# Performance work log

Measured on AMD Instinct MI355X. Metric: run time of the kernel, lower is better.

The kernel has to match this reference:

```python
import jax, jax.numpy as jnp
import numpy as np
from jax.ops import segment_sum, segment_max

N = 100_000          # nodes
E = 1_600_000        # directed edges (avg degree 16)
F_IN = 128           # raw node embedding dim
D = 64               # node_encoding
H = 4                # num_heads
GRAPH_LAYERS = 2
FLOW_ITERS = 10
COST_CONST = 1.0     # quadratic cost: c * f^2
NEG_SLOPE = 0.2      # GAT leaky-relu slope
EPS = 1e-9


def setup_inputs() -> dict:
    key = jax.random.key(0)
    ks = jax.random.split(key, 16)
    s = 0.05
    return {
        "demands": jax.random.normal(ks[0], (N, 1), jnp.float32),
        "node_embeddings": jax.random.normal(ks[1], (N, F_IN), jnp.float32),
        "edge_src": jax.random.randint(ks[2], (E,), 0, N),
        "edge_dst": jax.random.randint(ks[3], (E,), 0, N),
        # node encoder MLP (no hidden layers)
        "W_enc": jax.random.normal(ks[4], (F_IN + 1, D), jnp.float32) * s,
        "b_enc": jnp.zeros((D,), jnp.float32),
        # SparseGAT params (shared across graph_layers, matching AUTO_REUSE scope)
        "W_gat": jax.random.normal(ks[5], (H, D, D), jnp.float32) * s,
        "a_src_w": jax.random.normal(ks[6], (H, D), jnp.float32) * s,
        "a_dst_w": jax.random.normal(ks[7], (H, D), jnp.float32) * s,
        "b_gat": jnp.zeros((D,), jnp.float32),
        # Gate (GRU-style convex gate)
        "W_gx": jax.random.normal(ks[8], (D, D), jnp.float32) * s,
        "W_gh": jax.random.normal(ks[9], (D, D), jnp.float32) * s,
        "b_g": jnp.zeros((D,), jnp.float32),
        # decoder to 1 output feature
        "W_dec": jax.random.normal(ks[10], (D, 1), jnp.float32) * s,
        "b_dec": jnp.zeros((1,), jnp.float32),
    }


def _seg_softmax(e, seg, n):
    # numerically stable softmax over entries sharing the same segment (row)
    m = segment_max(e, seg, num_segments=n)
    ex = jnp.exp(e - m[seg])
    den = segment_sum(ex, seg, num_segments=n)
    return ex / (den[seg] + EPS)


def reference(demands, node_embeddings, edge_src, edge_dst,
              W_enc, b_enc, W_gat, a_src_w, a_dst_w, b_gat,
              W_gx, W_gh, b_g, W_dec, b_dec):
    loops = jnp.arange(N, dtype=edge_src.dtype)
    src_sl = jnp.concatenate([edge_src, loops])  # adj + I for GAT
    dst_sl = jnp.concatenate([edge_dst, loops])

    # node encoder: relu(concat([emb, demands]) @ W + b)
    h = jax.nn.relu(jnp.concatenate([node_embeddings, demands], axis=1) @ W_enc + b_enc)

    for _ in range(GRAPH_LAYERS):
        t = jnp.einsum('nd,hde->nhe', h, W_gat)              # [N,H,D]
        ss = jnp.einsum('nhe,he->nh', t, a_src_w)            # [N,H]
        sd = jnp.einsum('nhe,he->nh', t, a_dst_w)
        e = jax.nn.leaky_relu(ss[src_sl] + sd[dst_sl], NEG_SLOPE)  # [E+N,H]
        alpha = _seg_softmax(e, src_sl, N)                   # row-wise attn
        agg = segment_sum(alpha[:, :, None] * t[dst_sl], src_sl, num_segments=N)  # [N,H,D]
        nxt = jax.nn.relu(agg.mean(axis=1) + b_gat)          # average heads
        # gate: convex combination of new and previous state
        z = jax.nn.sigmoid(nxt @ W_gx + h @ W_gh + b_g)
        h = z * nxt + (1.0 - z) * h

    pred = h @ W_dec + b_dec                                 # [N,1]
    # flow_weight_pred = sparse.softmax(adj * pred_weights): row-broadcast then row softmax
    scores = pred[edge_src, 0]                               # [E]
    fw = _seg_softmax(scores, edge_src, N)                   # edge values of flow_weight_pred

    d0 = demands[:, 0]

    def body(_, fv):
        inflow = segment_sum(fv, edge_dst, num_segments=N)   # column sums (axis=0)
        adj_in = jax.nn.relu(inflow - d0)
        return fw * adj_in[edge_src]                         # row-broadcast multiply

    flow = jax.lax.fori_loop(0, FLOW_ITERS, body, fw)
    flow_cost = jnp.sum(COST_CONST * flow * flow)            # quadratic edge cost
    return flow_cost, flow, fw
```

## Files before the change

kernel.cpp:

```cpp
#include <hip/hip_runtime.h>


static constexpr int BLK      = 256;
static constexpr int SCAN_BLK = 1024;
static constexpr int CHUNK    = 4096;
static constexpr int LB       = 9;
static constexpr int BN       = 512;

__global__ void hist_kernel(const int* __restrict__ src, const int* __restrict__ dst,
                            int* __restrict__ counts, int E, int B, int nb, int M) {
    extern __shared__ int lh[];
    const int nbins = 2 * B;
    for (int i = threadIdx.x; i < 4 * nbins; i += blockDim.x) lh[i] = 0;
    __syncthreads();
    int* my = lh + (threadIdx.x >> 6) * nbins;
    int base = blockIdx.x * CHUNK;
    int end  = base + CHUNK < E ? base + CHUNK : E;
    int i4beg = base >> 2, i4end = end >> 2;
    for (int i = i4beg + threadIdx.x; i < i4end; i += blockDim.x) {
        int4 s4 = ((const int4*)src)[i];
        int4 d4 = ((const int4*)dst)[i];
        atomicAdd(&my[d4.x >> LB], 1); atomicAdd(&my[B + (s4.x >> LB)], 1);
        atomicAdd(&my[d4.y >> LB], 1); atomicAdd(&my[B + (s4.y >> LB)], 1);
        atomicAdd(&my[d4.z >> LB], 1); atomicAdd(&my[B + (s4.z >> LB)], 1);
        atomicAdd(&my[d4.w >> LB], 1); atomicAdd(&my[B + (s4.w >> LB)], 1);
    }
    if (blockIdx.x == (int)gridDim.x - 1 && threadIdx.x == 0) {
        for (int e = i4end << 2; e < end; ++e) {
            atomicAdd(&my[dst[e] >> LB], 1);
            atomicAdd(&my[B + (src[e] >> LB)], 1);
        }
    }
    __syncthreads();
    for (int i = threadIdx.x; i < nbins; i += blockDim.x) {
        int s = lh[i] + lh[nbins + i] + lh[2 * nbins + i] + lh[3 * nbins + i];
        if (i < B) counts[i * nb + blockIdx.x] = s;
        else       counts[M + (i - B) * nb + blockIdx.x] = s;
    }
}

__global__ void scan_block_kernel(int* __restrict__ data, int* __restrict__ blocksum, int M2) {
    __shared__ int lds[SCAN_BLK];
    int t = threadIdx.x;
    int i = blockIdx.x * SCAN_BLK + t;
    int v = (i < M2) ? data[i] : 0;
    lds[t] = v;
    __syncthreads();
    for (int off = 1; off < SCAN_BLK; off <<= 1) {
        int tmp = (t >= off) ? lds[t - off] : 0;
        __syncthreads();
        lds[t] += tmp;
        __syncthreads();
    }
    if (i < M2) data[i] = lds[t] - v;
    if (t == SCAN_BLK - 1) blocksum[blockIdx.x] = lds[t];
}

__global__ void scan_partials_kernel(const int* __restrict__ bsum, int* __restrict__ boff, int n) {
    __shared__ int lds[SCAN_BLK];
    __shared__ int carry_s;
    if (threadIdx.x == 0) carry_s = 0;
    __syncthreads();
    for (int base = 0; base < n; base += SCAN_BLK) {
        int i = base + threadIdx.x;
        int v = (i < n) ? bsum[i] : 0;
        lds[threadIdx.x] = v;
        __syncthreads();
        for (int off = 1; off < SCAN_BLK; off <<= 1) {
            int tmp = (threadIdx.x >= off) ? lds[threadIdx.x - off] : 0;
            __syncthreads();
            lds[threadIdx.x] += tmp;
            __syncthreads();
        }
        int incl = lds[threadIdx.x];
        int c = carry_s;
        if (i < n) boff[i] = c + incl - v;
        __syncthreads();
        if (threadIdx.x == SCAN_BLK - 1) carry_s = c + incl;
        __syncthreads();
    }
}

__global__ void fused_scatter_kernel(const int* __restrict__ src, const int* __restrict__ dst,
                                     const int* __restrict__ counts, const int* __restrict__ boff,
                                     unsigned* __restrict__ packed, unsigned short* __restrict__ psrc,
                                     int E, int B, int nb, int M) {
    extern __shared__ int loff[];
    int b = blockIdx.x;
    for (int i = threadIdx.x; i < B; i += blockDim.x) {
        int id  = i * nb + b;
        int id2 = M + i * nb + b;
        loff[i]     = counts[id]  + boff[id >> 10];
        loff[B + i] = counts[id2] + boff[id2 >> 10] - E;
    }
    __syncthreads();
    int base = b * CHUNK;
    int end  = base + CHUNK < E ? base + CHUNK : E;
    int i4beg = base >> 2, i4end = end >> 2;
    for (int i = i4beg + threadIdx.x; i < i4end; i += blockDim.x) {
        int4 s4 = ((const int4*)src)[i];
        int4 d4 = ((const int4*)dst)[i];
        #pragma unroll
        for (int k = 0; k < 4; ++k) {
            int s = (k == 0) ? s4.x : (k == 1) ? s4.y : (k == 2) ? s4.z : s4.w;
            int d = (k == 0) ? d4.x : (k == 1) ? d4.y : (k == 2) ? d4.z : d4.w;
            int pos = atomicAdd(&loff[d >> LB], 1);
            packed[pos] = (unsigned)s | ((unsigned)(d & (BN - 1)) << 17);
            int pos2 = atomicAdd(&loff[B + (s >> LB)], 1);
            psrc[pos2] = (unsigned short)(s & (BN - 1));
        }
    }
    if (b == (int)gridDim.x - 1 && threadIdx.x == 0) {
        for (int e = i4end << 2; e < end; ++e) {
            int s = src[e], d = dst[e];
            int pos = atomicAdd(&loff[d >> LB], 1);
            packed[pos] = (unsigned)s | ((unsigned)(d & (BN - 1)) << 17);
            int pos2 = atomicAdd(&loff[B + (s >> LB)], 1);
            psrc[pos2] = (unsigned short)(s & (BN - 1));
        }
    }
}

__global__ void count_src_kernel(const unsigned short* __restrict__ psrc,
                                 const int* __restrict__ counts, const int* __restrict__ boff,
                                 float2* __restrict__ rz0, int N, int E, int B, int nb, int M) {
    __shared__ int cnt[8 * BN];
    int t = threadIdx.x;
    for (int i = t; i < 8 * BN; i += blockDim.x) cnt[i] = 0;
    __syncthreads();
    int b = blockIdx.x;
    int id  = M + b * nb;
    int beg = counts[id] + boff[id >> 10] - E;
    int end;
    if (b + 1 < B) { int id2 = M + (b + 1) * nb; end = counts[id2] + boff[id2 >> 10] - E; }
    else end = E;
    int w = t >> 6;
    for (int e = beg + t; e < end; e += blockDim.x)
        atomicAdd(&cnt[(w << 9) + psrc[e]], 1);
    __syncthreads();
    int g = (b << LB) + t;
    if (t < BN && g < N) {
        int tot = 0;
        #pragma unroll
        for (int r = 0; r < 8; ++r) tot += cnt[(r << 9) + t];
        float v = 1.0f / ((float)tot + 1e-9f);
        rz0[g] = make_float2(v, v);
    }
}

__global__ void fine_sort_kernel(const unsigned* __restrict__ packed,
                                 const int* __restrict__ counts, const int* __restrict__ boff,
                                 int* __restrict__ csr_src, int* __restrict__ row_ptr,
                                 int N, int E, int B, int nb) {
    __shared__ int cnt[8 * BN];
    __shared__ int off[BN];
    int t = threadIdx.x;
    int b = blockIdx.x;
    for (int i = t; i < 8 * BN; i += blockDim.x) cnt[i] = 0;
    __syncthreads();
    int id  = b * nb;
    int beg = counts[id] + boff[id >> 10];
    int end;
    if (b + 1 < B) { int id2 = (b + 1) * nb; end = counts[id2] + boff[id2 >> 10]; }
    else end = E;
    int w = t >> 6;
    for (int e = beg + t; e < end; e += blockDim.x)
        atomicAdd(&cnt[(w << 9) + (packed[e] >> 17)], 1);
    __syncthreads();
    int tot = 0;
    {
        #pragma unroll
        for (int r = 0; r < 8; ++r) tot += cnt[(r << 9) + t];
        off[t] = tot;
    }
    __syncthreads();
    for (int s = 1; s < BN; s <<= 1) {
        int v = (t >= s) ? off[t - s] : 0;
        __syncthreads();
        off[t] += v;
        __syncthreads();
    }
    int excl = beg + off[t] - tot;
    {
        int g = (b << LB) + t;
        if (g < N) row_ptr[g] = excl;
        int base2 = excl;
        #pragma unroll
        for (int r = 0; r < 8; ++r) {
            int c = cnt[(r << 9) + t];
            cnt[(r << 9) + t] = base2;
            base2 += c;
        }
    }
    __syncthreads();
    for (int e = beg + t; e < end; e += blockDim.x) {
        unsigned v = packed[e];
        int pos = atomicAdd(&cnt[(w << 9) + (v >> 17)], 1);
        csr_src[pos] = (int)(v & 0x1FFFFu);
    }
    if (b == 0 && t == 0) row_ptr[N] = E;
}

__global__ void spmv_csr2_kernel(const int* __restrict__ row_ptr, const int* __restrict__ csr_src,
                                 const float2* __restrict__ rz_in, const float* __restrict__ d0,
                                 float2* __restrict__ rz_out, int N) {
    int tid = blockIdx.x * blockDim.x + threadIdx.x;
    int n = tid >> 1;
    if (n >= N) return;
    int half = tid & 1;
    int beg = row_ptr[n], end = row_ptr[n + 1];
    int mid = beg + ((end - beg + 1) >> 1);
    int lo = half ? mid : beg;
    int hi = half ? end : mid;
    float a0 = 0.0f, a1 = 0.0f;
    int j = lo;
    for (; j + 1 < hi; j += 2) {
        a0 += rz_in[csr_src[j]].x;
        a1 += rz_in[csr_src[j + 1]].x;
    }
    if (j < hi) a0 += rz_in[csr_src[j]].x;
    float a = a0 + a1;
    a += __shfl_xor(a, 1, 64);
    if (half == 0) {
        float inv = rz_in[n].y;
        float p = a - d0[n];
        p = p > 0.0f ? p : 0.0f;
        rz_out[n] = make_float2(p * inv, inv);
    }
}

__global__ void final_kernel(const int* __restrict__ src, const float2* __restrict__ rz,
                             float* __restrict__ flow, float* __restrict__ fw,
                             float* __restrict__ partials, int E) {
    int i = blockIdx.x * blockDim.x + threadIdx.x;
    int E4 = E >> 2;
    float f2 = 0.0f;
    if (i < E4) {
        int4 s4 = ((const int4*)src)[i];
        float2 a = rz[s4.x], b = rz[s4.y], c = rz[s4.z], d = rz[s4.w];
        int e = i << 2;
        flow[e] = a.x; flow[e + 1] = b.x; flow[e + 2] = c.x; flow[e + 3] = d.x;
        fw[e]   = a.y; fw[e + 1]   = b.y; fw[e + 2]   = c.y; fw[e + 3]   = d.y;
        f2 = a.x * a.x + b.x * b.x + c.x * c.x + d.x * d.x;
    }
    if (blockIdx.x == 0 && threadIdx.x == 0) {
        for (int e = E4 << 2; e < E; ++e) {
            float2 a = rz[src[e]];
            flow[e] = a.x; fw[e] = a.y;
            f2 += a.x * a.x;
        }
    }
    #pragma unroll
    for (int off = 32; off > 0; off >>= 1) f2 += __shfl_down(f2, off, 64);
    __shared__ float wsum[BLK / 64];
    int lane = threadIdx.x & 63, w = threadIdx.x >> 6;
    if (lane == 0) wsum[w] = f2;
    __syncthreads();
    if (threadIdx.x == 0) {
        float s = 0.0f;
        #pragma unroll
        for (int k = 0; k < BLK / 64; ++k) s += wsum[k];
        partials[blockIdx.x] = s;
    }
}

__global__ void reduce_cost_kernel(const float* __restrict__ partials, float* __restrict__ cost, int n) {
    float s = 0.0f;
    for (int i = threadIdx.x; i < n; i += blockDim.x) s += partials[i];
    #pragma unroll
    for (int off = 32; off > 0; off >>= 1) s += __shfl_down(s, off, 64);
    __shared__ float wsum[16];
    int lane = threadIdx.x & 63, w = threadIdx.x >> 6;
    if (lane == 0) wsum[w] = s;
    __syncthreads();
    if (threadIdx.x == 0) {
        float t = 0.0f;
        for (int k = 0; k < (int)(blockDim.x / 64); ++k) t += wsum[k];
        cost[0] = t;
    }
}

extern "C" void kernel_launch(void* const* d_in, const int* in_sizes, int n_in,
                              void* d_out, int out_size, void* d_ws, size_t ws_size,
                              hipStream_t stream) {
    const float* demands  = (const float*)d_in[0];
    const int*   edge_src = (const int*)d_in[2];
    const int*   edge_dst = (const int*)d_in[3];
    const int N = in_sizes[0];
    const int E = in_sizes[2];

    float* out  = (float*)d_out;
    float* cost = out;
    float* flow = out + 1;
    float* fw   = out + 1 + E;

    const int B   = (N + BN - 1) >> LB;
    const int nb  = (E + CHUNK - 1) / CHUNK;
    const int M   = B * nb;
    const int M2  = 2 * M;
    const int nbs = (M2 + SCAN_BLK - 1) / SCAN_BLK;
    const int gridF = ((E >> 2) + BLK - 1) / BLK;
    const int gridS = (2 * N + BLK - 1) / BLK;

    auto align16 = [](size_t x) { return (x + 15) & ~size_t(15); };
    char* ws = (char*)d_ws;
    size_t o = 0;
    float2*   rz0      = (float2*)(ws + o);   o += align16((size_t)N * 8);
    float2*   rz1      = (float2*)(ws + o);   o += align16((size_t)N * 8);
    int*      row_ptr  = (int*)(ws + o);      o += align16((size_t)(N + 1) * 4);
    int*      counts   = (int*)(ws + o);      o += align16((size_t)M2 * 4);
    int*      blocksum = (int*)(ws + o);      o += align16((size_t)nbs * 4);
    int*      blockoff = (int*)(ws + o);      o += align16((size_t)nbs * 4);
    unsigned* packed   = (unsigned*)(ws + o); o += align16((size_t)E * 4);
    unsigned short* psrc = (unsigned short*)(ws + o); o += align16((size_t)E * 2);
    int*      csr_src  = (int*)(ws + o);      o += align16((size_t)E * 4);
    float*    partials = (float*)(ws + o);    o += align16((size_t)gridF * 4);

    hist_kernel<<<nb, BLK, (size_t)(8 * B) * 4, stream>>>(edge_src, edge_dst, counts, E, B, nb, M);
    scan_block_kernel<<<nbs, SCAN_BLK, 0, stream>>>(counts, blocksum, M2);
    scan_partials_kernel<<<1, SCAN_BLK, 0, stream>>>(blocksum, blockoff, nbs);

    fused_scatter_kernel<<<nb, BLK, (size_t)(2 * B) * 4, stream>>>(
        edge_src, edge_dst, counts, blockoff, packed, psrc, E, B, nb, M);
    count_src_kernel<<<B, BN, 0, stream>>>(psrc, counts, blockoff, rz0, N, E, B, nb, M);
    fine_sort_kernel<<<B, BN, 0, stream>>>(packed, counts, blockoff, csr_src, row_ptr, N, E, B, nb);

    float2* r_cur = rz0;
    float2* r_nxt = rz1;
    for (int it = 0; it < 10; ++it) {
        spmv_csr2_kernel<<<gridS, BLK, 0, stream>>>(row_ptr, csr_src, r_cur, demands, r_nxt, N);
        float2* t = r_cur; r_cur = r_nxt; r_nxt = t;
    }

    final_kernel<<<gridF, BLK, 0, stream>>>(edge_src, r_cur, flow, fw, partials, E);
    reduce_cost_kernel<<<1, 1024, 0, stream>>>(partials, cost, gridF);
}
```

Before: 188.2 us.

## Fuse sort kernels, split SpMV rows four ways, fold cost reduction into final

Result: slower. 229.8 us (+22.1%).

```diff
diff --git a/kernel.cpp b/kernel.cpp
--- a/kernel.cpp
+++ b/kernel.cpp
@@ -6,6 +6,7 @@
 static constexpr int CHUNK    = 4096;
 static constexpr int LB       = 9;
 static constexpr int BN       = 512;
+
 
 __global__ void hist_kernel(const int* __restrict__ src, const int* __restrict__ dst,
                             int* __restrict__ counts, int E, int B, int nb, int M) {
@@ -56,10 +57,11 @@
     if (t == SCAN_BLK - 1) blocksum[blockIdx.x] = lds[t];
 }
 
-__global__ void scan_partials_kernel(const int* __restrict__ bsum, int* __restrict__ boff, int n) {
+__global__ void scan_partials_kernel(const int* __restrict__ bsum, int* __restrict__ boff,
+                                     int* __restrict__ ticket, int n) {
     __shared__ int lds[SCAN_BLK];
     __shared__ int carry_s;
-    if (threadIdx.x == 0) carry_s = 0;
+    if (threadIdx.x == 0) { carry_s = 0; ticket[0] = 0; }
     __syncthreads();
     for (int base = 0; base < n; base += SCAN_BLK) {
         int i = base + threadIdx.x;
@@ -121,58 +123,48 @@
     }
 }
 
-__global__ void count_src_kernel(const unsigned short* __restrict__ psrc,
-                                 const int* __restrict__ counts, const int* __restrict__ boff,
-                                 float2* __restrict__ rz0, int N, int E, int B, int nb, int M) {
+__global__ void bucket_kernel(const unsigned short* __restrict__ psrc,
+                              const unsigned* __restrict__ packed,
+                              const int* __restrict__ counts, const int* __restrict__ boff,
+                              float* __restrict__ invdeg, float* __restrict__ rA,
+                              int* __restrict__ csr_src, int* __restrict__ row_ptr,
+                              int N, int E, int B, int nb, int M) {
     __shared__ int cnt[8 * BN];
-    int t = threadIdx.x;
+    __shared__ int off[BN];
+    int t = threadIdx.x, b = blockIdx.x, w = t >> 6;
+    int g = (b << LB) + t;
     for (int i = t; i < 8 * BN; i += blockDim.x) cnt[i] = 0;
     __syncthreads();
-    int b = blockIdx.x;
-    int id  = M + b * nb;
+    int id = M + b * nb;
     int beg = counts[id] + boff[id >> 10] - E;
     int end;
     if (b + 1 < B) { int id2 = M + (b + 1) * nb; end = counts[id2] + boff[id2 >> 10] - E; }
     else end = E;
-    int w = t >> 6;
     for (int e = beg + t; e < end; e += blockDim.x)
         atomicAdd(&cnt[(w << 9) + psrc[e]], 1);
     __syncthreads();
-    int g = (b << LB) + t;
-    if (t < BN && g < N) {
+    if (g < N) {
         int tot = 0;
         #pragma unroll
         for (int r = 0; r < 8; ++r) tot += cnt[(r << 9) + t];
         float v = 1.0f / ((float)tot + 1e-9f);
-        rz0[g] = make_float2(v, v);
-    }
-}
-
-__global__ void fine_sort_kernel(const unsigned* __restrict__ packed,
-                                 const int* __restrict__ counts, const int* __restrict__ boff,
-                                 int* __restrict__ csr_src, int* __restrict__ row_ptr,
-                                 int N, int E, int B, int nb) {
-    __shared__ int cnt[8 * BN];
-    __shared__ int off[BN];
-    int t = threadIdx.x;
-    int b = blockIdx.x;
+        invdeg[g] = v;
+        rA[g] = v;
+    }
+    __syncthreads();
     for (int i = t; i < 8 * BN; i += blockDim.x) cnt[i] = 0;
     __syncthreads();
-    int id  = b * nb;
-    int beg = counts[id] + boff[id >> 10];
-    int end;
+    id = b * nb;
+    beg = counts[id] + boff[id >> 10];
     if (b + 1 < B) { int id2 = (b + 1) * nb; end = counts[id2] + boff[id2 >> 10]; }
     else end = E;
-    int w = t >> 6;
     for (int e = beg + t; e < end; e += blockDim.x)
         atomicAdd(&cnt[(w << 9) + (packed[e] >> 17)], 1);
     __syncthreads();
     int tot = 0;
-    {
-        #pragma unroll
-        for (int r = 0; r < 8; ++r) tot += cnt[(r << 9) + t];
-        off[t] = tot;
-    }
+    #pragma unroll
+    for (int r = 0; r < 8; ++r) tot += cnt[(r << 9) + t];
+    off[t] = tot;
     __syncthreads();
     for (int s = 1; s < BN; s <<= 1) {
         int v = (t >= s) ? off[t - s] : 0;
@@ -181,16 +173,11 @@
         __syncthreads();
     }
     int excl = beg + off[t] - tot;
+    if (g < N) row_ptr[g] = excl;
     {
-        int g = (b << LB) + t;
-        if (g < N) row_ptr[g] = excl;
         int base2 = excl;
         #pragma unroll
-        for (int r = 0; r < 8; ++r) {
-            int c = cnt[(r << 9) + t];
-            cnt[(r << 9) + t] = base2;
-            base2 += c;
-        }
+        for (int r = 0; r < 8; ++r) { int c = cnt[(r << 9) + t]; cnt[(r << 9) + t] = base2; base2 += c; }
     }
     __syncthreads();
     for (int e = beg + t; e < end; e += blockDim.x) {
@@ -201,53 +188,50 @@
     if (b == 0 && t == 0) row_ptr[N] = E;
 }
 
-__global__ void spmv_csr2_kernel(const int* __restrict__ row_ptr, const int* __restrict__ csr_src,
-                                 const float2* __restrict__ rz_in, const float* __restrict__ d0,
-                                 float2* __restrict__ rz_out, int N) {
+
+__global__ void spmv_q_kernel(const int* __restrict__ row_ptr, const int* __restrict__ csr_src,
+                              const float* __restrict__ r_in, const float* __restrict__ d0,
+                              const float* __restrict__ invdeg, float* __restrict__ r_out, int N) {
     int tid = blockIdx.x * blockDim.x + threadIdx.x;
-    int n = tid >> 1;
+    int n = tid >> 2;
     if (n >= N) return;
-    int half = tid & 1;
+    int q = tid & 3;
     int beg = row_ptr[n], end = row_ptr[n + 1];
-    int mid = beg + ((end - beg + 1) >> 1);
-    int lo = half ? mid : beg;
-    int hi = half ? end : mid;
-    float a0 = 0.0f, a1 = 0.0f;
-    int j = lo;
-    for (; j + 1 < hi; j += 2) {
-        a0 += rz_in[csr_src[j]].x;
-        a1 += rz_in[csr_src[j + 1]].x;
-    }
-    if (j < hi) a0 += rz_in[csr_src[j]].x;
-    float a = a0 + a1;
+    int len = end - beg;
+    int lo = beg + ((len * q) >> 2);
+    int hi = beg + ((len * (q + 1)) >> 2);
+    float a = 0.0f;
+    for (int j = lo; j < hi; ++j) a += r_in[csr_src[j]];
     a += __shfl_xor(a, 1, 64);
-    if (half == 0) {
-        float inv = rz_in[n].y;
+    a += __shfl_xor(a, 2, 64);
+    if (q == 0) {
         float p = a - d0[n];
         p = p > 0.0f ? p : 0.0f;
-        rz_out[n] = make_float2(p * inv, inv);
-    }
-}
-
-__global__ void final_kernel(const int* __restrict__ src, const float2* __restrict__ rz,
-                             float* __restrict__ flow, float* __restrict__ fw,
-                             float* __restrict__ partials, int E) {
+        r_out[n] = p * invdeg[n];
+    }
+}
+
+__global__ void final_kernel(const int* __restrict__ src, const float* __restrict__ r_fin,
+                             const float* __restrict__ invdeg, float* __restrict__ flow,
+                             float* __restrict__ fw, float* __restrict__ partials,
+                             int* __restrict__ ticket, float* __restrict__ cost, int E) {
     int i = blockIdx.x * blockDim.x + threadIdx.x;
     int E4 = E >> 2;
     float f2 = 0.0f;
     if (i < E4) {
         int4 s4 = ((const int4*)src)[i];
-        float2 a = rz[s4.x], b = rz[s4.y], c = rz[s4.z], d = rz[s4.w];
+        float a = r_fin[s4.x], b = r_fin[s4.y], c = r_fin[s4.z], d = r_fin[s4.w];
         int e = i << 2;
-        flow[e] = a.x; flow[e + 1] = b.x; flow[e + 2] = c.x; flow[e + 3] = d.x;
-        fw[e]   = a.y; fw[e + 1]   = b.y; fw[e + 2]   = c.y; fw[e + 3]   = d.y;
-        f2 = a.x * a.x + b.x * b.x + c.x * c.x + d.x * d.x;
+        flow[e] = a; flow[e + 1] = b; flow[e + 2] = c; flow[e + 3] = d;
+        fw[e] = invdeg[s4.x]; fw[e + 1] = invdeg[s4.y];
+        fw[e + 2] = invdeg[s4.z]; fw[e + 3] = invdeg[s4.w];
+        f2 = a * a + b * b + c * c + d * d;
     }
     if (blockIdx.x == 0 && threadIdx.x == 0) {
         for (int e = E4 << 2; e < E; ++e) {
-            float2 a = rz[src[e]];
-            flow[e] = a.x; fw[e] = a.y;
-            f2 += a.x * a.x;
+            float a = r_fin[src[e]];
+            flow[e] = a; fw[e] = invdeg[src[e]];
+            f2 += a * a;
         }
     }
     #pragma unroll
@@ -256,27 +240,32 @@
     int lane = threadIdx.x & 63, w = threadIdx.x >> 6;
     if (lane == 0) wsum[w] = f2;
     __syncthreads();
+    __shared__ bool amLast;
     if (threadIdx.x == 0) {
         float s = 0.0f;
         #pragma unroll
         for (int k = 0; k < BLK / 64; ++k) s += wsum[k];
         partials[blockIdx.x] = s;
-    }
-}
-
-__global__ void reduce_cost_kernel(const float* __restrict__ partials, float* __restrict__ cost, int n) {
-    float s = 0.0f;
-    for (int i = threadIdx.x; i < n; i += blockDim.x) s += partials[i];
-    #pragma unroll
-    for (int off = 32; off > 0; off >>= 1) s += __shfl_down(s, off, 64);
-    __shared__ float wsum[16];
-    int lane = threadIdx.x & 63, w = threadIdx.x >> 6;
-    if (lane == 0) wsum[w] = s;
-    __syncthreads();
-    if (threadIdx.x == 0) {
-        float t = 0.0f;
-        for (int k = 0; k < (int)(blockDim.x / 64); ++k) t += wsum[k];
-        cost[0] = t;
+        __threadfence();
+        int prev = atomicAdd(ticket, 1);
+        amLast = (prev == (int)gridDim.x - 1);
+    }
+    __syncthreads();
+    if (amLast) {
+        __threadfence();
+        float s = 0.0f;
+        for (int k = threadIdx.x; k < (int)gridDim.x; k += blockDim.x) s += partials[k];
+        #pragma unroll
+        for (int off = 32; off > 0; off >>= 1) s += __shfl_down(s, off, 64);
+        __shared__ float wsum2[BLK / 64];
+        if (lane == 0) wsum2[w] = s;
+        __syncthreads();
+        if (threadIdx.x == 0) {
+            float t2 = 0.0f;
+            #pragma unroll
+            for (int k = 0; k < BLK / 64; ++k) t2 += wsum2[k];
+            cost[0] = t2;
+        }
     }
 }
 
@@ -300,17 +289,19 @@
     const int M2  = 2 * M;
     const int nbs = (M2 + SCAN_BLK - 1) / SCAN_BLK;
     const int gridF = ((E >> 2) + BLK - 1) / BLK;
-    const int gridS = (2 * N + BLK - 1) / BLK;
+    const int gridS = (4 * N + BLK - 1) / BLK;
 
     auto align16 = [](size_t x) { return (x + 15) & ~size_t(15); };
     char* ws = (char*)d_ws;
     size_t o = 0;
-    float2*   rz0      = (float2*)(ws + o);   o += align16((size_t)N * 8);
-    float2*   rz1      = (float2*)(ws + o);   o += align16((size_t)N * 8);
+    float*    invdeg   = (float*)(ws + o);    o += align16((size_t)N * 4);
+    float*    rA       = (float*)(ws + o);    o += align16((size_t)N * 4);
+    float*    rB       = (float*)(ws + o);    o += align16((size_t)N * 4);
     int*      row_ptr  = (int*)(ws + o);      o += align16((size_t)(N + 1) * 4);
     int*      counts   = (int*)(ws + o);      o += align16((size_t)M2 * 4);
     int*      blocksum = (int*)(ws + o);      o += align16((size_t)nbs * 4);
     int*      blockoff = (int*)(ws + o);      o += align16((size_t)nbs * 4);
+    int*      ticket   = (int*)(ws + o);      o += align16(4);
     unsigned* packed   = (unsigned*)(ws + o); o += align16((size_t)E * 4);
     unsigned short* psrc = (unsigned short*)(ws + o); o += align16((size_t)E * 2);
     int*      csr_src  = (int*)(ws + o);      o += align16((size_t)E * 4);
@@ -318,20 +309,19 @@
 
     hist_kernel<<<nb, BLK, (size_t)(8 * B) * 4, stream>>>(edge_src, edge_dst, counts, E, B, nb, M);
     scan_block_kernel<<<nbs, SCAN_BLK, 0, stream>>>(counts, blocksum, M2);
-    scan_partials_kernel<<<1, SCAN_BLK, 0, stream>>>(blocksum, blockoff, nbs);
-
+    scan_partials_kernel<<<1, SCAN_BLK, 0, stream>>>(blocksum, blockoff, ticket, nbs);
     fused_scatter_kernel<<<nb, BLK, (size_t)(2 * B) * 4, stream>>>(
         edge_src, edge_dst, counts, blockoff, packed, psrc, E, B, nb, M);
-    count_src_kernel<<<B, BN, 0, stream>>>(psrc, counts, blockoff, rz0, N, E, B, nb, M);
-    fine_sort_kernel<<<B, BN, 0, stream>>>(packed, counts, blockoff, csr_src, row_ptr, N, E, B, nb);
-
-    float2* r_cur = rz0;
-    float2* r_nxt = rz1;
+    bucket_kernel<<<B, BN, 0, stream>>>(psrc, packed, counts, blockoff,
+                                        invdeg, rA, csr_src, row_ptr, N, E, B, nb, M);
+
+    float* r_cur = rA;
+    float* r_nxt = rB;
     for (int it = 0; it < 10; ++it) {
-        spmv_csr2_kernel<<<gridS, BLK, 0, stream>>>(row_ptr, csr_src, r_cur, demands, r_nxt, N);
-        float2* t = r_cur; r_cur = r_nxt; r_nxt = t;
-    }
-
-    final_kernel<<<gridF, BLK, 0, stream>>>(edge_src, r_cur, flow, fw, partials, E);
-    reduce_cost_kernel<<<1, 1024, 0, stream>>>(partials, cost, gridF);
-}
+        spmv_q_kernel<<<gridS, BLK, 0, stream>>>(row_ptr, csr_src, r_cur, demands, invdeg, r_nxt, N);
+        float* t = r_cur; r_cur = r_nxt; r_nxt = t;
+    }
+
+    final_kernel<<<gridF, BLK, 0, stream>>>(edge_src, r_cur, invdeg, flow, fw,
+                                            partials, ticket, cost, E);
+}
```
